# Kernel optimization log

Measured on AMD Instinct MI355X. Metric: run time of the kernel, lower is better.

The kernel has to match this reference:

```python
import jax, jax.numpy as jnp
import numpy as np

D_IN = 2048
FEATURES = 2048
BATCH = 4
SEQ = 2048


def setup_inputs() -> dict:
    key = jax.random.key(0)
    k1, k2 = jax.random.split(key)
    inputs = jax.random.normal(k1, (BATCH, SEQ, D_IN), dtype=jnp.float32)
    # lecun_normal-style init: std = 1/sqrt(fan_in)
    kernel = jax.random.normal(k2, (D_IN, FEATURES), dtype=jnp.float32) / np.sqrt(D_IN)
    return {"inputs": inputs, "kernel": kernel}


def reference(inputs, kernel):
    # Spectral normalization: divide kernel by its top singular value,
    # obtained from a full (thin) SVD, exactly as the flax module does.
    s = jnp.linalg.svd(kernel, full_matrices=False, compute_uv=False)
    kernel_n = kernel / s[0]
    # Dense projection: [..., x] @ [x, f] -> [..., f]
    return jnp.einsum('...x,xf->...f', inputs, kernel_n)
```

## Files before the change

### kernel.cpp

```cpp
#include <hip/hip_runtime.h>
#include <hip/hip_bf16.h>


typedef __attribute__((ext_vector_type(8))) _Float16 f16x8;
typedef __attribute__((ext_vector_type(8))) short   s16x8;
typedef __attribute__((ext_vector_type(4))) short   s16x4;
typedef __attribute__((ext_vector_type(4))) float   f32x4;

#define DEV __device__ __forceinline__

DEV unsigned short f2bf(float x) {
  unsigned u = __float_as_uint(x);
  unsigned r = (u + 0x7FFFu + ((u >> 16) & 1u)) >> 16;
  return (unsigned short)r;
}
DEV float bf2f(unsigned short b) { return __uint_as_float(((unsigned)b) << 16); }

DEV void gl_lds16(const void* g, void* l) {
  __builtin_amdgcn_global_load_lds((const __attribute__((address_space(1))) void*)g,
                                   (__attribute__((address_space(3))) void*)l,
                                   16, 0, 0);
}

template <bool F16IN, bool TRI>
__global__ __launch_bounds__(256, 2)
void gemm_bt(const char* __restrict__ Ag, const char* __restrict__ Bg,
             float* __restrict__ Cg, int M, int N, int K, int ksz,
             float cscale, const float* __restrict__ scale_ptr)
{
  __shared__ unsigned char smem[32768];
  const int tid  = threadIdx.x;
  const int lane = tid & 63;
  const int wid  = tid >> 6;

  const int q = (int)gridDim.x >> 3;
  const int wgid = ((int)blockIdx.x & 7) * q + ((int)blockIdx.x >> 3);
  int bm, bn;
  if constexpr (TRI) {
    const int nbm = M >> 7;
    int rem = wgid, i = 0;
    while (rem >= nbm - i) { rem -= nbm - i; ++i; }
    bm = i; bn = i + rem;
  } else {
    const int nbm = M >> 7;
    bm = wgid % nbm; bn = wgid / nbm;
  }
  const int m0 = bm << 7, n0 = bn << 7;

  const int kbeg = (int)blockIdx.y * ksz;
  const size_t plane = TRI ? ((size_t)gridDim.x << 14) : ((size_t)M * (size_t)N);
  float* __restrict__ Cmy = Cg + (size_t)blockIdx.y * plane;

  float scale = cscale;
  if (scale_ptr) scale *= scale_ptr[0];

  const f32x4 zero = {0.f, 0.f, 0.f, 0.f};
  f32x4 acc[4][4];
#pragma unroll
  for (int i = 0; i < 4; i++)
#pragma unroll
    for (int j = 0; j < 4; j++) acc[i][j] = zero;

  const int wr = wid >> 1, wc = wid & 1;
  const size_t rowstride = (size_t)K * 2;

  for (int k0 = kbeg; k0 < kbeg + ksz; k0 += 64) {
#pragma unroll
    for (int p = 0; p < 4; p++) {
      const int b   = (p << 12) + (wid << 10) + (lane << 4);
      const int row = b >> 7;
      const int scb = (b & 127) ^ ((row & 7) << 4);
      const size_t goff = (size_t)row * rowstride + (size_t)(k0 << 1) + (size_t)scb;
      gl_lds16(Ag + (size_t)m0 * rowstride + goff, smem + (p << 12) + (wid << 10));
      gl_lds16(Bg + (size_t)n0 * rowstride + goff, smem + 16384 + (p << 12) + (wid << 10));
    }
    __syncthreads();

#pragma unroll
    for (int kk = 0; kk < 2; kk++) {
      s16x8 a[4], b[4];
      const int kb = (kk << 6) + ((lane >> 4) << 4);
#pragma unroll
      for (int i = 0; i < 4; i++) {
        const int ar = (wr << 6) + (i << 4) + (lane & 15);
        const int br = (wc << 6) + (i << 4) + (lane & 15);
        a[i] = *(const s16x8*)(smem + ((((ar << 7) + kb)) ^ ((ar & 7) << 4)));
        b[i] = *(const s16x8*)(smem + 16384 + ((((br << 7) + kb)) ^ ((br & 7) << 4)));
      }
#pragma unroll
      for (int i = 0; i < 4; i++)
#pragma unroll
        for (int j = 0; j < 4; j++) {
          if constexpr (F16IN)
            acc[i][j] = __builtin_amdgcn_mfma_f32_16x16x32_f16(
                __builtin_bit_cast(f16x8, a[i]), __builtin_bit_cast(f16x8, b[j]),
                acc[i][j], 0, 0, 0);
          else
            acc[i][j] = __builtin_amdgcn_mfma_f32_16x16x32_bf16(
                a[i], b[j], acc[i][j], 0, 0, 0);
        }
    }
    __syncthreads();
  }

  const int lcol = (wc << 6) + (lane & 15);
  const int lrow = (wr << 6) + ((lane >> 4) << 2);
#pragma unroll
  for (int i = 0; i < 4; i++)
#pragma unroll
    for (int j = 0; j < 4; j++)
#pragma unroll
      for (int r = 0; r < 4; r++) {
        const int rr = lrow + (i << 4) + r;
        const int cc = lcol + (j << 4);
        const float v = acc[i][j][r] * scale;
        if constexpr (TRI)
          Cmy[((size_t)wgid << 14) + (rr << 7) + cc] = v;
        else
          Cmy[(size_t)(m0 + rr) * (size_t)N + (n0 + cc)] = v;
      }
}

__global__ __launch_bounds__(256, 2)
void reduce_sym(const float* __restrict__ P, unsigned short* __restrict__ o)
{
  __shared__ unsigned short tl[128][136];
  const int b = (int)blockIdx.x;
  int rem = b, i = 0;
  while (rem >= 16 - i) { rem -= 16 - i; ++i; }
  const int bm = i, bn = i + rem;
  const int t = threadIdx.x;
  const size_t PS = (size_t)136 << 14;
  const float* p = P + ((size_t)b << 14);

#pragma unroll
  for (int s = 0; s < 16; s++) {
    const int idx = (s << 10) + (t << 2);
    const int r = idx >> 7, c = idx & 127;
    f32x4 v = *(const f32x4*)(p + idx);
    v += *(const f32x4*)(p + PS + idx);
    v += *(const f32x4*)(p + 2 * PS + idx);
    v += *(const f32x4*)(p + 3 * PS + idx);
    s16x4 u;
#pragma unroll
    for (int e = 0; e < 4; e++) u[e] = (short)f2bf(v[e]);
    *(s16x4*)(o + (((size_t)(bm << 7) + r) << 11) + (bn << 7) + c) = u;
#pragma unroll
    for (int e = 0; e < 4; e++) tl[c + e][r] = (unsigned short)u[e];
  }
  __syncthreads();
  if (bm == bn) return;

#pragma unroll
  for (int pass = 0; pass < 4; pass++) {
    const int crw = (pass << 5) + (t >> 3);
    const int r0  = (t & 7) << 4;
    const s16x8 w0 = *(const s16x8*)(&tl[crw][r0]);
    const s16x8 w1 = *(const s16x8*)(&tl[crw][r0 + 8]);
    unsigned short* od = o + (((size_t)(bn << 7) + crw) << 11) + (bm << 7) + r0;
    *(s16x8*)(od)     = w0;
    *(s16x8*)(od + 8) = w1;
  }
}

__global__ __launch_bounds__(256)
void matvec4(const unsigned short* __restrict__ Cm,
             const float* __restrict__ vin, float* __restrict__ vout)
{
  const int row  = ((int)blockIdx.x << 2) + ((int)threadIdx.x >> 6);
  const int lane = threadIdx.x & 63;
  const unsigned short* crow = Cm + ((size_t)row << 11) + (lane << 5);
  const float* vp = vin + (lane << 7);
  float s0 = 0.f, s1 = 0.f, s2 = 0.f, s3 = 0.f;
#pragma unroll
  for (int u = 0; u < 4; u++) {
    const s16x8 cv = *(const s16x8*)(crow + (u << 3));
#pragma unroll
    for (int e = 0; e < 8; e++) {
      const float w = bf2f((unsigned short)cv[e]);
      const f32x4 vv = *(const f32x4*)(vp + (((u << 3) + e) << 2));
      s0 += w * vv[0]; s1 += w * vv[1]; s2 += w * vv[2]; s3 += w * vv[3];
    }
  }
#pragma unroll
  for (int d = 32; d > 0; d >>= 1) {
    s0 += __shfl_down(s0, d);
    s1 += __shfl_down(s1, d);
    s2 += __shfl_down(s2, d);
    s3 += __shfl_down(s3, d);
  }
  if (lane == 0) {
    float* o = vout + ((size_t)row << 2);
    o[0] = s0; o[1] = s1; o[2] = s2; o[3] = s3;
  }
}

__global__ void init_v(float* __restrict__ v) {
  const int i = (int)blockIdx.x * 256 + (int)threadIdx.x;
  unsigned h = (unsigned)i * 2654435761u;
  h ^= h >> 16; h *= 2246822519u; h ^= h >> 13;
  v[i] = (float)(h & 0xFFFFFFu) * (2.0f / 16777216.0f) - 1.0f;
}

__global__ __launch_bounds__(256)
void rayleigh_k(const float* __restrict__ vt, const float* __restrict__ y,
                float* __restrict__ sig)
{
  __shared__ float part[4][8];
  const int t = threadIdx.x, lane = t & 63, w = t >> 6;
  float num[4] = {0, 0, 0, 0}, den[4] = {0, 0, 0, 0};
  for (int i = t; i < 2048; i += 256) {
    const f32x4 a = *(const f32x4*)(vt + ((size_t)i << 2));
    const f32x4 b = *(const f32x4*)(y + ((size_t)i << 2));
#pragma unroll
    for (int j = 0; j < 4; j++) { num[j] += a[j] * b[j]; den[j] += a[j] * a[j]; }
  }
#pragma unroll
  for (int d = 32; d > 0; d >>= 1)
#pragma unroll
    for (int j = 0; j < 4; j++) {
      num[j] += __shfl_down(num[j], d);
      den[j] += __shfl_down(den[j], d);
    }
  if (lane == 0) {
#pragma unroll
    for (int j = 0; j < 4; j++) { part[w][j] = num[j]; part[w][j + 4] = den[j]; }
  }
  __syncthreads();
  if (t == 0) {
    float R = 0.f;
#pragma unroll
    for (int j = 0; j < 4; j++) {
      const float nj = part[0][j] + part[1][j] + part[2][j] + part[3][j];
      const float dj = part[0][j + 4] + part[1][j + 4] + part[2][j + 4] + part[3][j + 4];
      R = fmaxf(R, nj / dj);
    }
    const float sigma = 2.0f * powf(R, 0.03125f);
    sig[0] = 1.0f / sigma;
  }
}

__global__ __launch_bounds__(256)
void convert_f16(const float* __restrict__ in, _Float16* __restrict__ out) {
  const size_t i = (((size_t)blockIdx.x * 256) + threadIdx.x) << 3;
  const f32x4 a = *(const f32x4*)(in + i);
  const f32x4 b = *(const f32x4*)(in + i + 4);
  f16x8 o;
#pragma unroll
  for (int e = 0; e < 4; e++) { o[e] = (_Float16)a[e]; o[e + 4] = (_Float16)b[e]; }
  *(f16x8*)(out + i) = o;
}

__global__ __launch_bounds__(256)
void transpose_f16(const float* __restrict__ Kin, _Float16* __restrict__ KT) {
  __shared__ float tile[64][65];
  const int t = threadIdx.x;
  const int c = t & 63, rq = t >> 6;
  const int d0 = (int)blockIdx.x << 6, f0 = (int)blockIdx.y << 6;
#pragma unroll
  for (int p = 0; p < 16; p++) {
    const int rr = (p << 2) + rq;
    tile[rr][c] = Kin[(size_t)(d0 + rr) * 2048 + f0 + c];
  }
  __syncthreads();
#pragma unroll
  for (int p = 0; p < 16; p++) {
    const int fl = (p << 2) + rq;
    KT[(size_t)(f0 + fl) * 2048 + d0 + c] = (_Float16)tile[c][fl];
  }
}

extern "C" void kernel_launch(void* const* d_in, const int* in_sizes, int n_in,
                              void* d_out, int out_size, void* d_ws, size_t ws_size,
                              hipStream_t stream)
{
  (void)in_sizes; (void)n_in; (void)out_size; (void)ws_size;
  const float* X  = (const float*)d_in[0];
  const float* Km = (const float*)d_in[1];
  float* out = (float*)d_out;
  char* ws = (char*)d_ws;

  _Float16* KT  = (_Float16*)ws;
  unsigned short* buf0 = (unsigned short*)(ws + (8u << 20));
  unsigned short* buf1 = (unsigned short*)(ws + (16u << 20));
  float* P   = (float*)(ws + (24u << 20));
  _Float16* X16 = (_Float16*)(ws + (24u << 20));
  float* V0  = (float*)(ws + (58u << 20));
  float* V1  = V0 + 8192;
  float* sig = V1 + 8192;

  transpose_f16<<<dim3(32, 32), 256, 0, stream>>>(Km, KT);

  gemm_bt<true, true><<<dim3(136, 4), 256, 0, stream>>>(
      (const char*)KT, (const char*)KT, P, 2048, 2048, 2048, 512, 0.25f, nullptr);
  reduce_sym<<<136, 256, 0, stream>>>(P, buf0);

  unsigned short* src = buf0;
  unsigned short* dst = buf1;
  for (int s = 0; s < 4; s++) {
    gemm_bt<false, true><<<dim3(136, 4), 256, 0, stream>>>(
        (const char*)src, (const char*)src, P, 2048, 2048, 2048, 512, 1.0f, nullptr);
    reduce_sym<<<136, 256, 0, stream>>>(P, dst);
    unsigned short* t = src; src = dst; dst = t;
  }

  convert_f16<<<8192, 256, 0, stream>>>(X, X16);

  init_v<<<32, 256, 0, stream>>>(V0);
  const int T = 5;
  for (int it = 0; it < T; it++)
    matvec4<<<512, 256, 0, stream>>>(src, (it & 1) ? V1 : V0, (it & 1) ? V0 : V1);
  const float* vt = ((T - 1) & 1) ? V1 : V0;
  const float* yv = ((T - 1) & 1) ? V0 : V1;
  rayleigh_k<<<1, 256, 0, stream>>>(vt, yv, sig);

  gemm_bt<true, false><<<dim3(1024, 1), 256, 0, stream>>>(
      (const char*)X16, (const char*)KT, out, 8192, 2048, 2048, 2048, 1.0f, sig);
}
```

Before: 417.8 us.

## Rewrite GEMM as 256x256 tile, 8-wave, double-buffered LDS pipeline

Swaps the 128x128, 4-wave GEMM for a 256x256 tile kernel with 8 waves and 128 KB of LDS split into two buffers. Global-to-LDS loads for the next k-tile are interleaved with MFMA phases, using fine-grained vmcnt waits, barriers and s_setprio. Larger tiles cut global traffic per FLOP, and the software pipeline hides load latency. In exchange, the symmetric Gram GEMMs compute some lower-triangle 128 blocks that are then discarded, and the 128 KB LDS allocation limits occupancy.

```diff
diff --git a/kernel.cpp b/kernel.cpp
--- a/kernel.cpp
+++ b/kernel.cpp
@@ -8,6 +8,8 @@
 typedef __attribute__((ext_vector_type(4))) float   f32x4;
 
 #define DEV __device__ __forceinline__
+#define FENCE() asm volatile("" ::: "memory")
+#define BAR()   __builtin_amdgcn_s_barrier()
 
 DEV unsigned short f2bf(float x) {
   unsigned u = __float_as_uint(x);
@@ -22,103 +24,217 @@
                                    16, 0, 0);
 }
 
+template <int P>
+DEV void stage1(const char* Ag, const char* Bg, unsigned char* smem,
+                int tid, size_t rowstride, int m0, int n0, int kt, int buf)
+{
+  const int lb   = tid << 4;
+  const int rip  = lb >> 7;
+  const int colb = lb & 127;
+  const int scb  = colb ^ ((rip & 7) << 4);
+  if constexpr (P < 4) {
+    const int grow = (P << 6) + rip;
+    gl_lds16(Bg + (size_t)(n0 + grow) * rowstride + (size_t)kt * 2 + scb,
+             smem + (buf << 16) + 32768 + (P << 13) + lb);
+  } else {
+    const int grow = ((P - 4) << 6) + rip;
+    gl_lds16(Ag + (size_t)(m0 + grow) * rowstride + (size_t)kt * 2 + scb,
+             smem + (buf << 16) + ((P - 4) << 13) + lb);
+  }
+}
+
 template <bool F16IN, bool TRI>
-__global__ __launch_bounds__(256, 2)
-void gemm_bt(const char* __restrict__ Ag, const char* __restrict__ Bg,
+__global__ __launch_bounds__(512, 2)
+void gemm256(const char* __restrict__ Ag, const char* __restrict__ Bg,
              float* __restrict__ Cg, int M, int N, int K, int ksz,
              float cscale, const float* __restrict__ scale_ptr)
 {
-  __shared__ unsigned char smem[32768];
+  __shared__ unsigned char smem[131072];
   const int tid  = threadIdx.x;
   const int lane = tid & 63;
   const int wid  = tid >> 6;
 
-  const int q = (int)gridDim.x >> 3;
-  const int wgid = ((int)blockIdx.x & 7) * q + ((int)blockIdx.x >> 3);
   int bm, bn;
   if constexpr (TRI) {
-    const int nbm = M >> 7;
-    int rem = wgid, i = 0;
-    while (rem >= nbm - i) { rem -= nbm - i; ++i; }
+    int rem = (int)blockIdx.x, i = 0;
+    while (rem >= 8 - i) { rem -= 8 - i; ++i; }
     bm = i; bn = i + rem;
   } else {
-    const int nbm = M >> 7;
+    const int q = (int)gridDim.x >> 3;
+    const int wgid = ((int)blockIdx.x & 7) * q + ((int)blockIdx.x >> 3);
+    const int nbm = M >> 8;
     bm = wgid % nbm; bn = wgid / nbm;
   }
-  const int m0 = bm << 7, n0 = bn << 7;
+  const int m0 = bm << 8, n0 = bn << 8;
 
   const int kbeg = (int)blockIdx.y * ksz;
-  const size_t plane = TRI ? ((size_t)gridDim.x << 14) : ((size_t)M * (size_t)N);
-  float* __restrict__ Cmy = Cg + (size_t)blockIdx.y * plane;
+  const int NT   = ksz >> 6;
+  float* __restrict__ Cmy =
+      Cg + (size_t)blockIdx.y * (TRI ? ((size_t)136 << 14) : ((size_t)M * (size_t)N));
 
   float scale = cscale;
   if (scale_ptr) scale *= scale_ptr[0];
 
+  const size_t rowstride = (size_t)K * 2;
+
   const f32x4 zero = {0.f, 0.f, 0.f, 0.f};
-  f32x4 acc[4][4];
-#pragma unroll
-  for (int i = 0; i < 4; i++)
+  f32x4 acc[8][4];
+#pragma unroll
+  for (int i = 0; i < 8; i++)
 #pragma unroll
     for (int j = 0; j < 4; j++) acc[i][j] = zero;
 
-  const int wr = wid >> 1, wc = wid & 1;
-  const size_t rowstride = (size_t)K * 2;
-
-  for (int k0 = kbeg; k0 < kbeg + ksz; k0 += 64) {
-#pragma unroll
-    for (int p = 0; p < 4; p++) {
-      const int b   = (p << 12) + (wid << 10) + (lane << 4);
-      const int row = b >> 7;
-      const int scb = (b & 127) ^ ((row & 7) << 4);
-      const size_t goff = (size_t)row * rowstride + (size_t)(k0 << 1) + (size_t)scb;
-      gl_lds16(Ag + (size_t)m0 * rowstride + goff, smem + (p << 12) + (wid << 10));
-      gl_lds16(Bg + (size_t)n0 * rowstride + goff, smem + 16384 + (p << 12) + (wid << 10));
-    }
-    __syncthreads();
-
-#pragma unroll
-    for (int kk = 0; kk < 2; kk++) {
-      s16x8 a[4], b[4];
-      const int kb = (kk << 6) + ((lane >> 4) << 4);
-#pragma unroll
-      for (int i = 0; i < 4; i++) {
-        const int ar = (wr << 6) + (i << 4) + (lane & 15);
-        const int br = (wc << 6) + (i << 4) + (lane & 15);
-        a[i] = *(const s16x8*)(smem + ((((ar << 7) + kb)) ^ ((ar & 7) << 4)));
-        b[i] = *(const s16x8*)(smem + 16384 + ((((br << 7) + kb)) ^ ((br & 7) << 4)));
-      }
-#pragma unroll
-      for (int i = 0; i < 4; i++)
-#pragma unroll
-        for (int j = 0; j < 4; j++) {
-          if constexpr (F16IN)
-            acc[i][j] = __builtin_amdgcn_mfma_f32_16x16x32_f16(
-                __builtin_bit_cast(f16x8, a[i]), __builtin_bit_cast(f16x8, b[j]),
-                acc[i][j], 0, 0, 0);
-          else
-            acc[i][j] = __builtin_amdgcn_mfma_f32_16x16x32_bf16(
-                a[i], b[j], acc[i][j], 0, 0, 0);
+  auto rdA = [&](int cur, int i, int kk) -> s16x8 {
+    const int row = ((wid >> 2) << 7) + (i << 4) + (lane & 15);
+    const int kb  = (kk << 6) + ((lane >> 4) << 4);
+    return *(const s16x8*)(smem + (cur << 16) + (row << 7) + (kb ^ ((row & 7) << 4)));
+  };
+  auto rdB = [&](int cur, int j, int kk) -> s16x8 {
+    const int row = ((wid & 3) << 6) + (j << 4) + (lane & 15);
+    const int kb  = (kk << 6) + ((lane >> 4) << 4);
+    return *(const s16x8*)(smem + (cur << 16) + 32768 + (row << 7) + (kb ^ ((row & 7) << 4)));
+  };
+  auto MM = [&](const s16x8& a, const s16x8& b, f32x4 c) -> f32x4 {
+    if constexpr (F16IN)
+      return __builtin_amdgcn_mfma_f32_16x16x32_f16(
+          __builtin_bit_cast(f16x8, a), __builtin_bit_cast(f16x8, b), c, 0, 0, 0);
+    else
+      return __builtin_amdgcn_mfma_f32_16x16x32_bf16(a, b, c, 0, 0, 0);
+  };
+
+  stage1<0>(Ag, Bg, smem, tid, rowstride, m0, n0, kbeg, 0);
+  stage1<1>(Ag, Bg, smem, tid, rowstride, m0, n0, kbeg, 0);
+  stage1<2>(Ag, Bg, smem, tid, rowstride, m0, n0, kbeg, 0);
+  stage1<3>(Ag, Bg, smem, tid, rowstride, m0, n0, kbeg, 0);
+  stage1<4>(Ag, Bg, smem, tid, rowstride, m0, n0, kbeg, 0);
+  stage1<6>(Ag, Bg, smem, tid, rowstride, m0, n0, kbeg, 0);
+  stage1<5>(Ag, Bg, smem, tid, rowstride, m0, n0, kbeg, 0);
+  stage1<7>(Ag, Bg, smem, tid, rowstride, m0, n0, kbeg, 0);
+  asm volatile("s_waitcnt vmcnt(2)" ::: "memory");
+  BAR(); FENCE();
+
+  int cur = 0;
+  for (int t = 0; t < NT; ++t) {
+    const int nxt = cur ^ 1;
+    const int kn  = (t + 1 < NT) ? kbeg + ((t + 1) << 6) : kbeg;
+    s16x8 aq[4][2], bq[2][2];
+
+#pragma unroll
+    for (int i = 0; i < 4; i++)
+#pragma unroll
+      for (int kk = 0; kk < 2; kk++) aq[i][kk] = rdA(cur, i, kk);
+#pragma unroll
+    for (int j = 0; j < 2; j++)
+#pragma unroll
+      for (int kk = 0; kk < 2; kk++) bq[j][kk] = rdB(cur, j, kk);
+    stage1<0>(Ag, Bg, smem, tid, rowstride, m0, n0, kn, nxt);
+    stage1<1>(Ag, Bg, smem, tid, rowstride, m0, n0, kn, nxt);
+    FENCE(); BAR();
+    __builtin_amdgcn_s_setprio(1);
+#pragma unroll
+    for (int i = 0; i < 4; i++)
+#pragma unroll
+      for (int j = 0; j < 2; j++)
+#pragma unroll
+        for (int kk = 0; kk < 2; kk++)
+          acc[i][j] = MM(aq[i][kk], bq[j][kk], acc[i][j]);
+    __builtin_amdgcn_s_setprio(0);
+    FENCE(); BAR();
+
+#pragma unroll
+    for (int j = 0; j < 2; j++)
+#pragma unroll
+      for (int kk = 0; kk < 2; kk++) bq[j][kk] = rdB(cur, j + 2, kk);
+    stage1<2>(Ag, Bg, smem, tid, rowstride, m0, n0, kn, nxt);
+    stage1<3>(Ag, Bg, smem, tid, rowstride, m0, n0, kn, nxt);
+    FENCE(); BAR();
+    __builtin_amdgcn_s_setprio(1);
+#pragma unroll
+    for (int i = 0; i < 4; i++)
+#pragma unroll
+      for (int j = 0; j < 2; j++)
+#pragma unroll
+        for (int kk = 0; kk < 2; kk++)
+          acc[i][j + 2] = MM(aq[i][kk], bq[j][kk], acc[i][j + 2]);
+    __builtin_amdgcn_s_setprio(0);
+    asm volatile("s_waitcnt vmcnt(4)" ::: "memory");
+    BAR(); FENCE();
+
+#pragma unroll
+    for (int i = 0; i < 4; i++)
+#pragma unroll
+      for (int kk = 0; kk < 2; kk++) aq[i][kk] = rdA(cur, i + 4, kk);
+#pragma unroll
+    for (int j = 0; j < 2; j++)
+#pragma unroll
+      for (int kk = 0; kk < 2; kk++) bq[j][kk] = rdB(cur, j, kk);
+    stage1<4>(Ag, Bg, smem, tid, rowstride, m0, n0, kn, nxt);
+    stage1<6>(Ag, Bg, smem, tid, rowstride, m0, n0, kn, nxt);
+    FENCE(); BAR();
+    __builtin_amdgcn_s_setprio(1);
+#pragma unroll
+    for (int i = 0; i < 4; i++)
+#pragma unroll
+      for (int j = 0; j < 2; j++)
+#pragma unroll
+        for (int kk = 0; kk < 2; kk++)
+          acc[i + 4][j] = MM(aq[i][kk], bq[j][kk], acc[i + 4][j]);
+    __builtin_amdgcn_s_setprio(0);
+    FENCE(); BAR();
+
+#pragma unroll
+    for (int j = 0; j < 2; j++)
+#pragma unroll
+      for (int kk = 0; kk < 2; kk++) bq[j][kk] = rdB(cur, j + 2, kk);
+    stage1<5>(Ag, Bg, smem, tid, rowstride, m0, n0, kn, nxt);
+    stage1<7>(Ag, Bg, smem, tid, rowstride, m0, n0, kn, nxt);
+    FENCE(); BAR();
+    __builtin_amdgcn_s_setprio(1);
+#pragma unroll
+    for (int i = 0; i < 4; i++)
+#pragma unroll
+      for (int j = 0; j < 2; j++)
+#pragma unroll
+        for (int kk = 0; kk < 2; kk++)
+          acc[i + 4][j + 2] = MM(aq[i][kk], bq[j][kk], acc[i + 4][j + 2]);
+    __builtin_amdgcn_s_setprio(0);
+    asm volatile("s_waitcnt vmcnt(2)" ::: "memory");
+    BAR(); FENCE();
+
+    cur = nxt;
+  }
+
+  if constexpr (TRI) {
+    const int R128 = (bm << 1) + (wid >> 2);
+    const int C128 = (bn << 1) + ((wid & 3) >> 1);
+    if (R128 > C128) return;
+    const int t128 = R128 * 16 - (R128 * (R128 - 1)) / 2 + (C128 - R128);
+    const int coff = ((wid & 1) << 6);
+    float* base = Cmy + ((size_t)t128 << 14);
+#pragma unroll
+    for (int i = 0; i < 8; i++)
+#pragma unroll
+      for (int j = 0; j < 4; j++)
+#pragma unroll
+        for (int r = 0; r < 4; r++) {
+          const int rl = (i << 4) + ((lane >> 4) << 2) + r;
+          const int cl = coff + (j << 4) + (lane & 15);
+          base[(rl << 7) + cl] = acc[i][j][r] * scale;
         }
-    }
-    __syncthreads();
-  }
-
-  const int lcol = (wc << 6) + (lane & 15);
-  const int lrow = (wr << 6) + ((lane >> 4) << 2);
-#pragma unroll
-  for (int i = 0; i < 4; i++)
-#pragma unroll
-    for (int j = 0; j < 4; j++)
-#pragma unroll
-      for (int r = 0; r < 4; r++) {
-        const int rr = lrow + (i << 4) + r;
-        const int cc = lcol + (j << 4);
-        const float v = acc[i][j][r] * scale;
-        if constexpr (TRI)
-          Cmy[((size_t)wgid << 14) + (rr << 7) + cc] = v;
-        else
-          Cmy[(size_t)(m0 + rr) * (size_t)N + (n0 + cc)] = v;
-      }
+  } else {
+    const int wm = m0 + ((wid >> 2) << 7);
+    const int wn = n0 + ((wid & 3) << 6);
+#pragma unroll
+    for (int i = 0; i < 8; i++)
+#pragma unroll
+      for (int j = 0; j < 4; j++)
+#pragma unroll
+        for (int r = 0; r < 4; r++) {
+          const int rr = wm + (i << 4) + ((lane >> 4) << 2) + r;
+          const int cc = wn + (j << 4) + (lane & 15);
+          Cmy[(size_t)rr * (size_t)N + cc] = acc[i][j][r] * scale;
+        }
+  }
 }
 
 __global__ __launch_bounds__(256, 2)
@@ -291,14 +407,14 @@
 
   transpose_f16<<<dim3(32, 32), 256, 0, stream>>>(Km, KT);
 
-  gemm_bt<true, true><<<dim3(136, 4), 256, 0, stream>>>(
+  gemm256<true, true><<<dim3(36, 4), 512, 0, stream>>>(
       (const char*)KT, (const char*)KT, P, 2048, 2048, 2048, 512, 0.25f, nullptr);
   reduce_sym<<<136, 256, 0, stream>>>(P, buf0);
 
   unsigned short* src = buf0;
   unsigned short* dst = buf1;
   for (int s = 0; s < 4; s++) {
-    gemm_bt<false, true><<<dim3(136, 4), 256, 0, stream>>>(
+    gemm256<false, true><<<dim3(36, 4), 512, 0, stream>>>(
         (const char*)src, (const char*)src, P, 2048, 2048, 2048, 512, 1.0f, nullptr);
     reduce_sym<<<136, 256, 0, stream>>>(P, dst);
     unsigned short* t = src; src = dst; dst = t;
@@ -314,6 +430,6 @@
   const float* yv = ((T - 1) & 1) ? V0 : V1;
   rayleigh_k<<<1, 256, 0, stream>>>(vt, yv, sig);
 
-  gemm_bt<true, false><<<dim3(1024, 1), 256, 0, stream>>>(
+  gemm256<true, false><<<dim3(256, 1), 512, 0, stream>>>(
       (const char*)X16, (const char*)KT, out, 8192, 2048, 2048, 2048, 1.0f, sig);
 }
```

New measurement: 391.9 us. -6.2%, faster.
